# Kernel optimization log

Hardware: AMD Instinct MI355X
Metric: run time of the kernel (lower is better)

The kernel has to match this reference:

```python
import jax, jax.numpy as jnp
import numpy as np
from jax import lax

# ---- config (mirrors cfg) ----
NUM_LEVELS = 4
DS = 2            # DS_FACTOR
T = 16            # TILE_SIZE
SR = 4            # SEARCH_RADIUS
PADD = 1
SW = 0.1          # SPATIAL_WEIGHT
GR = 2            # GAUSS_RADIUS
SIGMA = 1.0
SS = 2 * (SR + PADD) + 1      # 11: padded search grid
SSC = 2 * SR + 1              # 9: cropped search grid
WIN = T + 2 * (SR + PADD)     # 26: gathered window per tile

# ---- subpixel-refinement quadratic-fit filters (from __init__) ----
F_A11 = jnp.asarray(np.array([[1,-2,1],[2,-4,2],[1,-2,1]], np.float32) / 4.0)
F_A22 = jnp.asarray(np.array([[1,2,1],[-2,-4,-2],[1,2,1]], np.float32) / 4.0)
F_A12 = jnp.asarray(np.array([[1,0,-1],[0,0,0],[-1,0,1]], np.float32) / 4.0)
F_B1  = jnp.asarray(np.array([[-1,0,1],[-2,0,2],[-1,0,1]], np.float32) / 8.0)
F_B2  = jnp.asarray(np.array([[-1,-2,-1],[0,0,0],[1,2,1]], np.float32) / 8.0)
F_C   = jnp.asarray(np.array([[-1,2,-1],[2,12,2],[-1,2,-1]], np.float32) / 16.0)


def _gauss_kernel():
    ws = 2 * GR + 1
    ax = np.arange(ws, dtype=np.float32) - GR
    g = np.exp(-(ax ** 2) / (2.0 * SIGMA ** 2))
    k = np.outer(g, g)
    k = k / k.sum()
    return jnp.asarray(k, jnp.float32)


def _pyramid(x):
    """Gaussian pyramid: depthwise gaussian blur + avg-pool(ds) per level."""
    k = _gauss_kernel()[None, None]  # OIHW, C=1
    pad = (2 * GR + 1 - 1) // 2
    pyr = [x]
    for _ in range(NUM_LEVELS - 1):
        y = lax.conv_general_dilated(x, k, (1, 1), [(pad, pad), (pad, pad)],
                                     dimension_numbers=('NCHW', 'OIHW', 'NCHW'))
        n, c, h, w = y.shape
        x = y.reshape(n, c, h // DS, DS, w // DS, DS).mean(axis=(3, 5))
        pyr.append(x)
    return pyr


def _sdist_map():
    ax = (np.arange(SS, dtype=np.float32) - (SR + PADD)) / float(SS)
    return jnp.asarray(ax[:, None] ** 2 + ax[None, :] ** 2, jnp.float32)


def _step(init_offset, src, dst):
    """One pyramid-level block-matching step + subpixel refine."""
    n, nth, ntw, _ = init_offset.shape
    H, W = src.shape[2], src.shape[3]
    oy = jnp.round(init_offset[..., 0]).astype(jnp.int32)
    ox = jnp.round(init_offset[..., 1]).astype(jnp.int32)
    base_y = (jnp.arange(nth, dtype=jnp.int32) * T)[None, :, None]
    base_x = (jnp.arange(ntw, dtype=jnp.int32) * T)[None, None, :]
    y0 = base_y + oy - (SR + PADD)
    x0 = base_x + ox - (SR + PADD)
    Y = jnp.clip(y0[..., None] + jnp.arange(WIN), 0, H - 1)
    X = jnp.clip(x0[..., None] + jnp.arange(WIN), 0, W - 1)
    nidx = jnp.arange(n)[:, None, None, None, None]
    window = dst[:, 0][nidx, Y[..., :, None], X[..., None, :]]
    # source tiles [n,nth,ntw,T,T]
    src_t = src[:, 0].reshape(n, nth, T, ntw, T).transpose(0, 1, 3, 2, 4)
    # all SSxSS candidate tiles from the window (static slide indices)
    sl = jnp.arange(SS)[:, None] + jnp.arange(T)[None, :]  # [SS,T]
    cand = window[:, :, :, sl[:, None, :, None], sl[None, :, None, :]]  # [n,nth,ntw,SS,SS,T,T]
    adist = jnp.mean((cand - src_t[:, :, :, None, None]) ** 2, axis=(-2, -1))
    dist_full = adist + SW * _sdist_map()  # [n,nth,ntw,SS,SS]
    dist = dist_full[:, :, :, PADD:-PADD, PADD:-PADD].reshape(n, nth, ntw, SSC * SSC)
    min_dist = jnp.min(dist, axis=3)
    pk = jnp.argmin(dist, axis=3)
    py = pk // SSC
    px = pk % SSC
    offset = init_offset + jnp.stack([(py - SR).astype(jnp.float32),
                                      (px - SR).astype(jnp.float32)], axis=3)
    # RegionSelection: 3x3 neighborhood of dist_full around (py+PADD, px+PADD)
    ry = (py + PADD)[..., None] + jnp.arange(-1, 2)
    rx = (px + PADD)[..., None] + jnp.arange(-1, 2)
    tyi = jnp.arange(nth)[None, :, None, None, None]
    txi = jnp.arange(ntw)[None, None, :, None, None]
    yreg = dist_full[nidx, tyi, txi, ry[..., :, None], rx[..., None, :]]  # [n,nth,ntw,3,3]
    s = lambda f: jnp.sum(f * yreg, axis=(-2, -1))
    a11 = jax.nn.relu(s(F_A11))
    a22 = jax.nn.relu(s(F_A22))
    a12 = s(F_A12)
    b1 = s(F_B1)
    b2 = s(F_B2)
    det = a11 * a22 - a12 ** 2
    a12z = jnp.where(det < 0, jnp.zeros_like(a12), a12)
    mu_x = -(a22 * b1 - a12z * b2) / det
    mu_y = -(a11 * b2 - a12z * b1) / det
    mu_len = jnp.sqrt(mu_y ** 2 + mu_x ** 2)
    dx = jnp.where(mu_len < 1.0, mu_x, jnp.zeros_like(mu_x))
    dy = jnp.where(mu_len < 1.0, mu_y, jnp.zeros_like(mu_y))
    offset = offset.at[..., 0].add(dy).at[..., 1].add(dx)
    return offset, min_dist


def _inherit(prev_offset, nth, ntw, H, W):
    typ = jnp.arange(nth) // DS
    txp = jnp.arange(ntw) // DS
    off = DS * prev_offset[:, typ[:, None], txp[None, :], :]
    iy = (jnp.arange(nth, dtype=jnp.float32) * T)[None, :, None]
    ix = (jnp.arange(ntw, dtype=jnp.float32) * T)[None, None, :]
    dy = jnp.clip(off[..., 0] + iy, 0.0, float(H - T)) - iy
    dx = jnp.clip(off[..., 1] + ix, 0.0, float(W - T)) - ix
    return jnp.round(jnp.stack([dy, dx], axis=3))


def _align(src, dst):
    ps = _pyramid(src)
    pd = _pyramid(dst)
    offset = None
    min_dist = None
    for level in range(NUM_LEVELS - 1, -1, -1):
        s, d = ps[level], pd[level]
        n, _, h, w = s.shape
        nth = int(np.ceil(h / T))
        ntw = int(np.ceil(w / T))
        if level == NUM_LEVELS - 1:
            init = jnp.zeros((n, nth, ntw, 2), jnp.float32)
        else:
            init = _inherit(offset, nth, ntw, h, w)
        offset, min_dist = _step(init, s, d)
    # nearest-neighbor upsample by TILE_SIZE to per-pixel maps
    pixel_off = jnp.repeat(jnp.repeat(offset, T, axis=1), T, axis=2)   # [n,H,W,2]
    pixel_dist = jnp.repeat(jnp.repeat(min_dist, T, axis=1), T, axis=2)  # [n,H,W]
    return pixel_off, pixel_dist


def setup_inputs() -> dict:
    key = jax.random.key(0)
    k1, k2 = jax.random.split(key)
    src = jax.random.uniform(k1, (4, 1, 512, 512), jnp.float32)
    dst = jax.random.uniform(k2, (4, 1, 512, 512), jnp.float32)
    return {"src": src, "dst": dst}


def reference(src, dst):
    return _align(src, dst)
```

## Files before the change

kernel.cpp:

```cpp
#include <hip/hip_runtime.h>


#define NB 4
#define NPIX (NB * 512 * 512)

constexpr float H6[6] = {
    0.027244342f, 0.149345013f, 0.323410645f,
    0.323410645f, 0.149345013f, 0.027244342f
};

__global__ void __launch_bounds__(256, 4)
pyramid_kernel(const float* __restrict__ src, const float* __restrict__ dst,
               float* __restrict__ ws) {
    __shared__ float smem[5520];
    float* patch = smem;
    float* tmpH1 = smem + 3840;
    float* l1    = smem;
    float* tmpH2 = smem + 784;
    float* l2    = smem + 1120;
    float* tmpH3 = smem + 1264;

    float* sL1 = ws;
    float* dL1 = sL1 + 4 * 65536;
    float* sL2 = dL1 + 4 * 65536;
    float* dL2 = sL2 + 4 * 16384;
    float* sL3 = dL2 + 4 * 16384;
    float* dL3 = sL3 + 4 * 4096;

    const int bx = blockIdx.x, by = blockIdx.y, z = blockIdx.z;
    const int t = threadIdx.x;
    const float* in = (z < 4) ? (src + (size_t)z * 262144) : (dst + (size_t)(z - 4) * 262144);
    float* oL1 = ((z < 4) ? sL1 : dL1) + (size_t)(z & 3) * 65536;
    float* oL2 = ((z < 4) ? sL2 : dL2) + (size_t)(z & 3) * 16384;
    float* oL3 = ((z < 4) ? sL3 : dL3) + (size_t)(z & 3) * 4096;

    {
        const int oy = by * 32 - 14, ox = bx * 32 - 14;
        for (int idx = t; idx < 3600; idx += 256) {
            int r = idx / 60, c = idx - r * 60;
            int gy = oy + r, gx = ox + c;
            float v = 0.f;
            if ((unsigned)gy < 512u && (unsigned)gx < 512u) v = in[gy * 512 + gx];
            patch[r * 64 + c] = v;
        }
    }
    __syncthreads();
    for (int idx = t; idx < 1680; idx += 256) {
        int r = idx / 28, v = idx - r * 28;
        const float* p = &patch[r * 64 + 2 * v];
        float a = 0.f;
        #pragma unroll
        for (int bq = 0; bq < 6; ++bq) a = fmaf(H6[bq], p[bq], a);
        tmpH1[r * 28 + v] = a;
    }
    __syncthreads();
    {
        const int oy = by * 16 - 6, ox = bx * 16 - 6;
        for (int idx = t; idx < 784; idx += 256) {
            int u = idx / 28, v = idx - u * 28;
            float a = 0.f;
            int y1 = oy + u, x1 = ox + v;
            if ((unsigned)y1 < 256u && (unsigned)x1 < 256u) {
                #pragma unroll
                for (int bq = 0; bq < 6; ++bq) a = fmaf(H6[bq], tmpH1[(2 * u + bq) * 28 + v], a);
            }
            l1[u * 28 + v] = a;
        }
    }
    __syncthreads();
    {
        int u = t >> 4, v = t & 15;
        oL1[(by * 16 + u) * 256 + bx * 16 + v] = l1[(6 + u) * 28 + 6 + v];
    }
    for (int idx = t; idx < 336; idx += 256) {
        int r = idx / 12, v = idx - r * 12;
        const float* p = &l1[r * 28 + 2 * v];
        float a = 0.f;
        #pragma unroll
        for (int bq = 0; bq < 6; ++bq) a = fmaf(H6[bq], p[bq], a);
        tmpH2[r * 12 + v] = a;
    }
    __syncthreads();
    {
        const int oy = by * 8 - 2, ox = bx * 8 - 2;
        if (t < 144) {
            int u = t / 12, v = t - u * 12;
            float a = 0.f;
            int y2 = oy + u, x2 = ox + v;
            if ((unsigned)y2 < 128u && (unsigned)x2 < 128u) {
                #pragma unroll
                for (int bq = 0; bq < 6; ++bq) a = fmaf(H6[bq], tmpH2[(2 * u + bq) * 12 + v], a);
            }
            l2[u * 12 + v] = a;
        }
    }
    __syncthreads();
    if (t < 64) {
        int u = t >> 3, v = t & 7;
        oL2[(by * 8 + u) * 128 + bx * 8 + v] = l2[(2 + u) * 12 + 2 + v];
    } else if (t < 112) {
        int idx = t - 64;
        int r = idx >> 2, v = idx & 3;
        const float* p = &l2[r * 12 + 2 * v];
        float a = 0.f;
        #pragma unroll
        for (int bq = 0; bq < 6; ++bq) a = fmaf(H6[bq], p[bq], a);
        tmpH3[r * 4 + v] = a;
    }
    __syncthreads();
    if (t < 16) {
        int u = t >> 2, v = t & 3;
        float a = 0.f;
        #pragma unroll
        for (int bq = 0; bq < 6; ++bq) a = fmaf(H6[bq], tmpH3[(2 * u + bq) * 4 + v], a);
        oL3[(by * 4 + u) * 64 + bx * 4 + v] = a;
    }
}

template<bool FULL>
__device__ __forceinline__ void do_level(const float* __restrict__ simg,
                                         const float* __restrict__ dimg, int H,
                                         int ty, int tx, float pary, float parx, bool first,
                                         float* win, float* st, float* dist, int lt,
                                         float& roy, float& rox, float& rod) {
    constexpr int NL = FULL ? 256 : 128;

    float dyf = 0.f, dxf = 0.f;
    if (!first) {
        float iy = (float)(ty * 16), ix = (float)(tx * 16);
        dyf = rintf(fminf(fmaxf(2.f * pary + iy, 0.f), (float)(H - 16)) - iy);
        dxf = rintf(fminf(fmaxf(2.f * parx + ix, 0.f), (float)(H - 16)) - ix);
    }
    const int ioy = (int)dyf, iox = (int)dxf;
    const int y0 = ty * 16 + ioy - 5;
    const int x0 = tx * 16 + iox - 5;

    for (int idx = lt; idx < 676; idx += NL) {
        int r = idx / 26, c = idx - r * 26;
        int gy = min(max(y0 + r, 0), H - 1);
        int gx = min(max(x0 + c, 0), H - 1);
        win[r * 28 + c] = dimg[gy * H + gx];
    }
    if (lt < 64) {
        int r = lt >> 2, q = lt & 3;
        const float4* srow = (const float4*)(simg + (size_t)(ty * 16 + r) * H + tx * 16);
        ((float4*)&st[r * 16])[q] = srow[q];
    }
    __syncthreads();

    const int dy = FULL ? (lt >> 4) : (lt >> 3);
    if (dy < 11) {
        float acc[11];
        #pragma unroll
        for (int q = 0; q < 11; ++q) acc[q] = 0.f;
        constexpr int ROWS = FULL ? 1 : 2;
        #pragma unroll
        for (int rr = 0; rr < ROWS; ++rr) {
            const int i = FULL ? (lt & 15) : ((lt & 7) * 2 + rr);
            float w[28], s[16];
            const float4* wp = (const float4*)&win[(dy + i) * 28];
            #pragma unroll
            for (int q = 0; q < 7; ++q) ((float4*)w)[q] = wp[q];
            const float4* sp = (const float4*)&st[i * 16];
            #pragma unroll
            for (int q = 0; q < 4; ++q) ((float4*)s)[q] = sp[q];
            #pragma unroll
            for (int dx = 0; dx < 11; ++dx) {
                #pragma unroll
                for (int j = 0; j < 16; ++j) {
                    float d = w[dx + j] - s[j];
                    acc[dx] = fmaf(d, d, acc[dx]);
                }
            }
        }
        constexpr int MMAX = FULL ? 8 : 4;
        #pragma unroll
        for (int m = 1; m <= MMAX; m <<= 1) {
            #pragma unroll
            for (int dx = 0; dx < 11; ++dx) acc[dx] += __shfl_xor(acc[dx], m);
        }
        const bool leader = FULL ? ((lt & 15) == 0) : ((lt & 7) == 0);
        if (leader) {
            float ay = (float)(dy - 5) * (1.f / 11.f);
            #pragma unroll
            for (int dx = 0; dx < 11; ++dx) {
                float ax = (float)(dx - 5) * (1.f / 11.f);
                dist[dy * 11 + dx] = acc[dx] * (1.f / 256.f) + 0.1f * (ay * ay + ax * ax);
            }
        }
    }
    __syncthreads();

    const int l = lt & 63;
    float bv; int bk;
    {
        int k = l;
        int py = k / 9, px = k - (k / 9) * 9;
        bv = dist[(py + 1) * 11 + (px + 1)]; bk = k;
        k = l + 64;
        if (k < 81) {
            py = k / 9; px = k - (k / 9) * 9;
            float d = dist[(py + 1) * 11 + (px + 1)];
            if (d < bv) { bv = d; bk = k; }
        }
    }
    #pragma unroll
    for (int m = 1; m <= 32; m <<= 1) {
        float ov = __shfl_xor(bv, m);
        int   ok = __shfl_xor(bk, m);
        if (ov < bv || (ov == bv && ok < bk)) { bv = ov; bk = ok; }
    }
    {
        int py = bk / 9, px = bk - (bk / 9) * 9;
        float y00 = dist[(py + 0) * 11 + (px + 0)], y01 = dist[(py + 0) * 11 + (px + 1)], y02 = dist[(py + 0) * 11 + (px + 2)];
        float y10 = dist[(py + 1) * 11 + (px + 0)], y11 = dist[(py + 1) * 11 + (px + 1)], y12 = dist[(py + 1) * 11 + (px + 2)];
        float y20 = dist[(py + 2) * 11 + (px + 0)], y21 = dist[(py + 2) * 11 + (px + 1)], y22 = dist[(py + 2) * 11 + (px + 2)];

        float a11 = (y00 - 2.f * y01 + y02 + 2.f * y10 - 4.f * y11 + 2.f * y12 + y20 - 2.f * y21 + y22) * 0.25f;
        a11 = fmaxf(a11, 0.f);
        float a22 = (y00 + 2.f * y01 + y02 - 2.f * y10 - 4.f * y11 - 2.f * y12 + y20 + 2.f * y21 + y22) * 0.25f;
        a22 = fmaxf(a22, 0.f);
        float a12 = (y00 - y02 - y20 + y22) * 0.25f;
        float b1  = (-y00 + y02 - 2.f * y10 + 2.f * y12 - y20 + y22) * 0.125f;
        float b2  = (-y00 - 2.f * y01 - y02 + y20 + 2.f * y21 + y22) * 0.125f;

        float det  = a11 * a22 - a12 * a12;
        float a12z = (det < 0.f) ? 0.f : a12;
        float mu_x = -(a22 * b1 - a12z * b2) / det;
        float mu_y = -(a11 * b2 - a12z * b1) / det;
        float mu_len = sqrtf(mu_x * mu_x + mu_y * mu_y);
        float addx = (mu_len < 1.f) ? mu_x : 0.f;
        float addy = (mu_len < 1.f) ? mu_y : 0.f;

        roy = dyf + (float)(py - 4) + addy;
        rox = dxf + (float)(px - 4) + addx;
        rod = bv;
    }
}

__global__ void __launch_bounds__(256, 4)
step_chain_kernel(const float* __restrict__ src, const float* __restrict__ dst,
                  const float* __restrict__ ws, float* __restrict__ out) {
    __shared__ float winS[2][26 * 28];
    __shared__ float stS[2][256];
    __shared__ float distS[2][128];

    const float* sL1 = ws;
    const float* dL1 = sL1 + 4 * 65536;
    const float* sL2 = dL1 + 4 * 65536;
    const float* dL2 = sL2 + 4 * 16384;
    const float* sL3 = dL2 + 4 * 16384;
    const float* dL3 = sL3 + 4 * 4096;

    const int gid = blockIdx.x;
    const int b   = gid >> 8;
    const int ty1 = (gid >> 4) & 15;
    const int tx1 = gid & 15;
    const int t    = threadIdx.x;
    const int slot = t >> 7;
    const int s_t  = t & 127;

    const float* s0 = src + (size_t)b * 262144; const float* d0 = dst + (size_t)b * 262144;
    const float* s1 = sL1 + (size_t)b * 65536;  const float* d1 = dL1 + (size_t)b * 65536;
    const float* s2 = sL2 + (size_t)b * 16384;  const float* d2 = dL2 + (size_t)b * 16384;
    const float* s3 = sL3 + (size_t)b * 4096;   const float* d3 = dL3 + (size_t)b * 4096;

    float oy, ox, od;
    do_level<true>(s3, d3,  64, ty1 >> 2, tx1 >> 2, 0.f, 0.f, true,
                   winS[0], stS[0], distS[0], t, oy, ox, od);
    do_level<true>(s2, d2, 128, ty1 >> 1, tx1 >> 1, oy, ox, false,
                   winS[0], stS[0], distS[0], t, oy, ox, od);
    do_level<true>(s1, d1, 256, ty1,      tx1,      oy, ox, false,
                   winS[0], stS[0], distS[0], t, oy, ox, od);
    const float s1y = oy, s1x = ox;

    #pragma unroll
    for (int half = 0; half < 2; ++half) {
        const int ty0 = 2 * ty1 + half, tx0 = 2 * tx1 + slot;
        do_level<false>(s0, d0, 512, ty0, tx0, s1y, s1x, false,
                        winS[slot], stS[slot], distS[slot], s_t, oy, ox, od);
        int r = s_t >> 3, c = (s_t & 7) * 2;
        int pyy = ty0 * 16 + r, pxx = tx0 * 16 + c;
        size_t pi = ((size_t)(b * 512 + pyy)) * 512 + pxx;
        float2 o; o.x = oy; o.y = ox;
        ((float2*)out)[pi]     = o;
        ((float2*)out)[pi + 1] = o;
        float2 dd; dd.x = od; dd.y = od;
        *(float2*)(out + (size_t)NPIX * 2 + pi) = dd;
    }
}

extern "C" void kernel_launch(void* const* d_in, const int* in_sizes, int n_in,
                              void* d_out, int out_size, void* d_ws, size_t ws_size,
                              hipStream_t stream) {
    const float* src = (const float*)d_in[0];
    const float* dst = (const float*)d_in[1];
    float* out = (float*)d_out;
    float* ws  = (float*)d_ws;

    hipLaunchKernelGGL(pyramid_kernel, dim3(16, 16, 8), dim3(256), 0, stream, src, dst, ws);
    hipLaunchKernelGGL(step_chain_kernel, dim3(1024), dim3(256), 0, stream, src, dst, ws, out);
}
```

Baseline: 112.3 us.

## Process four level-0 tiles concurrently with 512-thread blocks

Doubles the step-chain block to 512 threads so the four finest-level tiles under each level-1 tile are matched at the same time by four 128-thread slots, instead of two slots each looping over two halves. Shared memory is laid out as one flat array with per-slot windows, and the level template is parameterised by thread count. The goal is to remove the serial second pass at the finest level. In exchange, the coarse levels leave more threads idle, and launch_bounds(512,4) tightens the per-thread register budget, which may cause spills in the unrolled SSD loop.

```diff
diff --git a/kernel.cpp b/kernel.cpp
--- a/kernel.cpp
+++ b/kernel.cpp
@@ -117,13 +117,14 @@
     }
 }
 
-template<bool FULL>
+template<int NL>
 __device__ __forceinline__ void do_level(const float* __restrict__ simg,
                                          const float* __restrict__ dimg, int H,
                                          int ty, int tx, float pary, float parx, bool first,
                                          float* win, float* st, float* dist, int lt,
                                          float& roy, float& rox, float& rod) {
-    constexpr int NL = FULL ? 256 : 128;
+    constexpr int ROWS = (NL == 128) ? 2 : 1;
+    constexpr int G    = (NL == 128) ? 8 : 16;
 
     float dyf = 0.f, dxf = 0.f;
     if (!first) {
@@ -148,15 +149,14 @@
     }
     __syncthreads();
 
-    const int dy = FULL ? (lt >> 4) : (lt >> 3);
+    const int dy = lt / G;
     if (dy < 11) {
         float acc[11];
         #pragma unroll
         for (int q = 0; q < 11; ++q) acc[q] = 0.f;
-        constexpr int ROWS = FULL ? 1 : 2;
         #pragma unroll
         for (int rr = 0; rr < ROWS; ++rr) {
-            const int i = FULL ? (lt & 15) : ((lt & 7) * 2 + rr);
+            const int i = (NL == 128) ? ((lt & 7) * 2 + rr) : (lt & 15);
             float w[28], s[16];
             const float4* wp = (const float4*)&win[(dy + i) * 28];
             #pragma unroll
@@ -173,14 +173,12 @@
                 }
             }
         }
-        constexpr int MMAX = FULL ? 8 : 4;
-        #pragma unroll
-        for (int m = 1; m <= MMAX; m <<= 1) {
+        #pragma unroll
+        for (int m = 1; m <= G / 2; m <<= 1) {
             #pragma unroll
             for (int dx = 0; dx < 11; ++dx) acc[dx] += __shfl_xor(acc[dx], m);
         }
-        const bool leader = FULL ? ((lt & 15) == 0) : ((lt & 7) == 0);
-        if (leader) {
+        if ((lt & (G - 1)) == 0) {
             float ay = (float)(dy - 5) * (1.f / 11.f);
             #pragma unroll
             for (int dx = 0; dx < 11; ++dx) {
@@ -238,12 +236,10 @@
     }
 }
 
-__global__ void __launch_bounds__(256, 4)
+__global__ void __launch_bounds__(512, 4)
 step_chain_kernel(const float* __restrict__ src, const float* __restrict__ dst,
                   const float* __restrict__ ws, float* __restrict__ out) {
-    __shared__ float winS[2][26 * 28];
-    __shared__ float stS[2][256];
-    __shared__ float distS[2][128];
+    __shared__ float smem[4448];
 
     const float* sL1 = ws;
     const float* dL1 = sL1 + 4 * 65536;
@@ -260,34 +256,38 @@
     const int slot = t >> 7;
     const int s_t  = t & 127;
 
+    float* win0  = smem;
+    float* st0   = smem + 2912;
+    float* dist0 = smem + 3936;
+    float* winH  = smem + slot * 728;
+    float* stH   = smem + 2912 + slot * 256;
+    float* distH = smem + 3936 + slot * 128;
+
     const float* s0 = src + (size_t)b * 262144; const float* d0 = dst + (size_t)b * 262144;
     const float* s1 = sL1 + (size_t)b * 65536;  const float* d1 = dL1 + (size_t)b * 65536;
     const float* s2 = sL2 + (size_t)b * 16384;  const float* d2 = dL2 + (size_t)b * 16384;
     const float* s3 = sL3 + (size_t)b * 4096;   const float* d3 = dL3 + (size_t)b * 4096;
 
     float oy, ox, od;
-    do_level<true>(s3, d3,  64, ty1 >> 2, tx1 >> 2, 0.f, 0.f, true,
-                   winS[0], stS[0], distS[0], t, oy, ox, od);
-    do_level<true>(s2, d2, 128, ty1 >> 1, tx1 >> 1, oy, ox, false,
-                   winS[0], stS[0], distS[0], t, oy, ox, od);
-    do_level<true>(s1, d1, 256, ty1,      tx1,      oy, ox, false,
-                   winS[0], stS[0], distS[0], t, oy, ox, od);
-    const float s1y = oy, s1x = ox;
-
-    #pragma unroll
-    for (int half = 0; half < 2; ++half) {
-        const int ty0 = 2 * ty1 + half, tx0 = 2 * tx1 + slot;
-        do_level<false>(s0, d0, 512, ty0, tx0, s1y, s1x, false,
-                        winS[slot], stS[slot], distS[slot], s_t, oy, ox, od);
-        int r = s_t >> 3, c = (s_t & 7) * 2;
-        int pyy = ty0 * 16 + r, pxx = tx0 * 16 + c;
-        size_t pi = ((size_t)(b * 512 + pyy)) * 512 + pxx;
-        float2 o; o.x = oy; o.y = ox;
-        ((float2*)out)[pi]     = o;
-        ((float2*)out)[pi + 1] = o;
-        float2 dd; dd.x = od; dd.y = od;
-        *(float2*)(out + (size_t)NPIX * 2 + pi) = dd;
-    }
+    do_level<512>(s3, d3,  64, ty1 >> 2, tx1 >> 2, 0.f, 0.f, true,
+                  win0, st0, dist0, t, oy, ox, od);
+    do_level<512>(s2, d2, 128, ty1 >> 1, tx1 >> 1, oy, ox, false,
+                  win0, st0, dist0, t, oy, ox, od);
+    do_level<512>(s1, d1, 256, ty1,      tx1,      oy, ox, false,
+                  win0, st0, dist0, t, oy, ox, od);
+
+    const int ty0 = 2 * ty1 + (slot >> 1), tx0 = 2 * tx1 + (slot & 1);
+    do_level<128>(s0, d0, 512, ty0, tx0, oy, ox, false,
+                  winH, stH, distH, s_t, oy, ox, od);
+
+    int r = s_t >> 3, c = (s_t & 7) * 2;
+    int pyy = ty0 * 16 + r, pxx = tx0 * 16 + c;
+    size_t pi = ((size_t)(b * 512 + pyy)) * 512 + pxx;
+    float2 o; o.x = oy; o.y = ox;
+    ((float2*)out)[pi]     = o;
+    ((float2*)out)[pi + 1] = o;
+    float2 dd; dd.x = od; dd.y = od;
+    *(float2*)(out + (size_t)NPIX * 2 + pi) = dd;
 }
 
 extern "C" void kernel_launch(void* const* d_in, const int* in_sizes, int n_in,
@@ -299,5 +299,5 @@
     float* ws  = (float*)d_ws;
 
     hipLaunchKernelGGL(pyramid_kernel, dim3(16, 16, 8), dim3(256), 0, stream, src, dst, ws);
-    hipLaunchKernelGGL(step_chain_kernel, dim3(1024), dim3(256), 0, stream, src, dst, ws, out);
+    hipLaunchKernelGGL(step_chain_kernel, dim3(1024), dim3(512), 0, stream, src, dst, ws, out);
 }
```

Measured after the change: 117.4 us. +4.5%, slower.

## Prefetch all source tiles upfront and batch level-0 window loads and SSD

Applied to the files above, without the earlier changes.

Splits the per-level routine into window loading, SSD distance and argmin/refine phases. All source tiles (levels 3, 2, 1 and four level-0 tiles) are preloaded into shared memory at kernel start, so those global loads overlap instead of being serialized inside each level. For level 0, both halves' windows are loaded together and their SSD maps are computed before either argmin, removing one round of load/sync latency. Shared memory grows to about 24KB per block, which may reduce occupancy below the four blocks per CU that the launch bounds target.

```diff
diff --git a/kernel.cpp b/kernel.cpp
--- a/kernel.cpp
+++ b/kernel.cpp
@@ -117,37 +117,28 @@
     }
 }
 
-template<bool FULL>
-__device__ __forceinline__ void do_level(const float* __restrict__ simg,
-                                         const float* __restrict__ dimg, int H,
-                                         int ty, int tx, float pary, float parx, bool first,
-                                         float* win, float* st, float* dist, int lt,
-                                         float& roy, float& rox, float& rod) {
-    constexpr int NL = FULL ? 256 : 128;
-
-    float dyf = 0.f, dxf = 0.f;
-    if (!first) {
-        float iy = (float)(ty * 16), ix = (float)(tx * 16);
-        dyf = rintf(fminf(fmaxf(2.f * pary + iy, 0.f), (float)(H - 16)) - iy);
-        dxf = rintf(fminf(fmaxf(2.f * parx + ix, 0.f), (float)(H - 16)) - ix);
-    }
-    const int ioy = (int)dyf, iox = (int)dxf;
-    const int y0 = ty * 16 + ioy - 5;
-    const int x0 = tx * 16 + iox - 5;
-
+__device__ __forceinline__ void inherit_off(int ty, int tx, int H,
+                                            float pary, float parx,
+                                            float& dyf, float& dxf) {
+    float iy = (float)(ty * 16), ix = (float)(tx * 16);
+    dyf = rintf(fminf(fmaxf(2.f * pary + iy, 0.f), (float)(H - 16)) - iy);
+    dxf = rintf(fminf(fmaxf(2.f * parx + ix, 0.f), (float)(H - 16)) - ix);
+}
+
+template<int NL>
+__device__ __forceinline__ void load_win(const float* __restrict__ dimg, int H,
+                                         int y0, int x0, float* win, int lt) {
     for (int idx = lt; idx < 676; idx += NL) {
         int r = idx / 26, c = idx - r * 26;
         int gy = min(max(y0 + r, 0), H - 1);
         int gx = min(max(x0 + c, 0), H - 1);
         win[r * 28 + c] = dimg[gy * H + gx];
     }
-    if (lt < 64) {
-        int r = lt >> 2, q = lt & 3;
-        const float4* srow = (const float4*)(simg + (size_t)(ty * 16 + r) * H + tx * 16);
-        ((float4*)&st[r * 16])[q] = srow[q];
-    }
-    __syncthreads();
-
+}
+
+template<bool FULL>
+__device__ __forceinline__ void ssd_dist(const float* win, const float* st,
+                                         float* dist, int lt) {
     const int dy = FULL ? (lt >> 4) : (lt >> 3);
     if (dy < 11) {
         float acc[11];
@@ -189,8 +180,11 @@
             }
         }
     }
-    __syncthreads();
-
+}
+
+__device__ __forceinline__ void argmin_refine(const float* dist, int lt,
+                                              float dyf, float dxf,
+                                              float& roy, float& rox, float& rod) {
     const int l = lt & 63;
     float bv; int bk;
     {
@@ -241,9 +235,7 @@
 __global__ void __launch_bounds__(256, 4)
 step_chain_kernel(const float* __restrict__ src, const float* __restrict__ dst,
                   const float* __restrict__ ws, float* __restrict__ out) {
-    __shared__ float winS[2][26 * 28];
-    __shared__ float stS[2][256];
-    __shared__ float distS[2][128];
+    __shared__ float smem[6072];
 
     const float* sL1 = ws;
     const float* dL1 = sL1 + 4 * 65536;
@@ -260,32 +252,99 @@
     const int slot = t >> 7;
     const int s_t  = t & 127;
 
+    float* win_c = smem;
+    float* dist_c = smem + 3640;
+    float* winA  = smem + 728 + (2 * slot + 0) * 728;
+    float* winB  = smem + 728 + (2 * slot + 1) * 728;
+    float* distA = smem + 3768 + (2 * slot + 0) * 128;
+    float* distB = smem + 3768 + (2 * slot + 1) * 128;
+    float* stL3 = smem + 4280;
+    float* stL2 = smem + 4536;
+    float* stL1 = smem + 4792;
+    float* st0  = smem + 5048;
+
     const float* s0 = src + (size_t)b * 262144; const float* d0 = dst + (size_t)b * 262144;
     const float* s1 = sL1 + (size_t)b * 65536;  const float* d1 = dL1 + (size_t)b * 65536;
     const float* s2 = sL2 + (size_t)b * 16384;  const float* d2 = dL2 + (size_t)b * 16384;
     const float* s3 = sL3 + (size_t)b * 4096;   const float* d3 = dL3 + (size_t)b * 4096;
 
+    {
+        const int it = t & 63, r = it >> 2, q = t & 3;
+        const int c = t >> 6;
+        const int ty0 = 2 * ty1 + (c >> 1), tx0 = 2 * tx1 + (c & 1);
+        const float4* p0 = (const float4*)(s0 + (size_t)(ty0 * 16 + r) * 512 + tx0 * 16);
+        ((float4*)&st0[c * 256 + r * 16])[q] = p0[q];
+        if (t < 64) {
+            const float4* p = (const float4*)(s3 + (size_t)((ty1 >> 2) * 16 + r) * 64 + (tx1 >> 2) * 16);
+            ((float4*)&stL3[r * 16])[q] = p[q];
+        } else if (t < 128) {
+            const float4* p = (const float4*)(s2 + (size_t)((ty1 >> 1) * 16 + r) * 128 + (tx1 >> 1) * 16);
+            ((float4*)&stL2[r * 16])[q] = p[q];
+        } else if (t < 192) {
+            const float4* p = (const float4*)(s1 + (size_t)(ty1 * 16 + r) * 256 + tx1 * 16);
+            ((float4*)&stL1[r * 16])[q] = p[q];
+        }
+    }
+
     float oy, ox, od;
-    do_level<true>(s3, d3,  64, ty1 >> 2, tx1 >> 2, 0.f, 0.f, true,
-                   winS[0], stS[0], distS[0], t, oy, ox, od);
-    do_level<true>(s2, d2, 128, ty1 >> 1, tx1 >> 1, oy, ox, false,
-                   winS[0], stS[0], distS[0], t, oy, ox, od);
-    do_level<true>(s1, d1, 256, ty1,      tx1,      oy, ox, false,
-                   winS[0], stS[0], distS[0], t, oy, ox, od);
-    const float s1y = oy, s1x = ox;
-
-    #pragma unroll
-    for (int half = 0; half < 2; ++half) {
-        const int ty0 = 2 * ty1 + half, tx0 = 2 * tx1 + slot;
-        do_level<false>(s0, d0, 512, ty0, tx0, s1y, s1x, false,
-                        winS[slot], stS[slot], distS[slot], s_t, oy, ox, od);
-        int r = s_t >> 3, c = (s_t & 7) * 2;
-        int pyy = ty0 * 16 + r, pxx = tx0 * 16 + c;
+    {
+        load_win<256>(d3, 64, (ty1 >> 2) * 16 - 5, (tx1 >> 2) * 16 - 5, win_c, t);
+        __syncthreads();
+        ssd_dist<true>(win_c, stL3, dist_c, t);
+        __syncthreads();
+        argmin_refine(dist_c, t, 0.f, 0.f, oy, ox, od);
+    }
+    {
+        float dyf, dxf; inherit_off(ty1 >> 1, tx1 >> 1, 128, oy, ox, dyf, dxf);
+        load_win<256>(d2, 128, (ty1 >> 1) * 16 + (int)dyf - 5, (tx1 >> 1) * 16 + (int)dxf - 5, win_c, t);
+        __syncthreads();
+        ssd_dist<true>(win_c, stL2, dist_c, t);
+        __syncthreads();
+        argmin_refine(dist_c, t, dyf, dxf, oy, ox, od);
+    }
+    {
+        float dyf, dxf; inherit_off(ty1, tx1, 256, oy, ox, dyf, dxf);
+        load_win<256>(d1, 256, ty1 * 16 + (int)dyf - 5, tx1 * 16 + (int)dxf - 5, win_c, t);
+        __syncthreads();
+        ssd_dist<true>(win_c, stL1, dist_c, t);
+        __syncthreads();
+        argmin_refine(dist_c, t, dyf, dxf, oy, ox, od);
+    }
+
+    const int tyA = 2 * ty1,     txA = 2 * tx1 + slot;
+    const int tyB = 2 * ty1 + 1, txB = 2 * tx1 + slot;
+    float dyfA, dxfA, dyfB, dxfB;
+    inherit_off(tyA, txA, 512, oy, ox, dyfA, dxfA);
+    inherit_off(tyB, txB, 512, oy, ox, dyfB, dxfB);
+    load_win<128>(d0, 512, tyA * 16 + (int)dyfA - 5, txA * 16 + (int)dxfA - 5, winA, s_t);
+    load_win<128>(d0, 512, tyB * 16 + (int)dyfB - 5, txB * 16 + (int)dxfB - 5, winB, s_t);
+    __syncthreads();
+    ssd_dist<false>(winA, st0 + (0 * 2 + slot) * 256, distA, s_t);
+    __syncthreads();
+    ssd_dist<false>(winB, st0 + (1 * 2 + slot) * 256, distB, s_t);
+    __syncthreads();
+
+    const int r = s_t >> 3, c2 = (s_t & 7) * 2;
+    {
+        float oyA, oxA, odA;
+        argmin_refine(distA, s_t, dyfA, dxfA, oyA, oxA, odA);
+        int pyy = tyA * 16 + r, pxx = txA * 16 + c2;
         size_t pi = ((size_t)(b * 512 + pyy)) * 512 + pxx;
-        float2 o; o.x = oy; o.y = ox;
+        float2 o; o.x = oyA; o.y = oxA;
         ((float2*)out)[pi]     = o;
         ((float2*)out)[pi + 1] = o;
-        float2 dd; dd.x = od; dd.y = od;
+        float2 dd; dd.x = odA; dd.y = odA;
+        *(float2*)(out + (size_t)NPIX * 2 + pi) = dd;
+    }
+    {
+        float oyB, oxB, odB;
+        argmin_refine(distB, s_t, dyfB, dxfB, oyB, oxB, odB);
+        int pyy = tyB * 16 + r, pxx = txB * 16 + c2;
+        size_t pi = ((size_t)(b * 512 + pyy)) * 512 + pxx;
+        float2 o; o.x = oyB; o.y = oxB;
+        ((float2*)out)[pi]     = o;
+        ((float2*)out)[pi + 1] = o;
+        float2 dd; dd.x = odB; dd.y = odB;
         *(float2*)(out + (size_t)NPIX * 2 + pi) = dd;
     }
 }
```

New measurement: 111.1 us. No clear change (-1.0%).
